# Kernel optimization log

Measured on AMD Instinct MI355X. Metric: run time of the kernel, lower is better.

## Reference

```python
import jax, jax.numpy as jnp
import numpy as np

B, L, C = 16, 4096, 32
D = 512
W = 24                  # rolling window
LAGS = [3, 5, 7]
MAXLEN = 5000
EPS = 1e-5


def setup_inputs() -> dict:
    key = jax.random.key(0)
    ks = jax.random.split(key, 8)
    return {
        "x": jax.random.normal(ks[0], (B, L, C), jnp.float32),
        "conv_w": jax.random.normal(ks[1], (D, C * (5 + len(LAGS)), 3), jnp.float32) * 0.05,
        "conv_b": jnp.zeros((D,), jnp.float32),
        "learned_pe": jax.random.normal(ks[2], (1, MAXLEN, D), jnp.float32) * (1.0 / np.sqrt(D)),
        "tape_pos": jax.random.normal(ks[3], (MAXLEN, D), jnp.float32) * 0.02,
        "tproj_w": jax.random.normal(ks[4], (D, D), jnp.float32) * 0.02,
        "tproj_b": jnp.zeros((D,), jnp.float32),
        "mixer_w": jax.random.normal(ks[5], (D, 2 * D), jnp.float32) * 0.02,
        "mixer_b": jnp.zeros((D,), jnp.float32),
        "g_c": jnp.ones((D,), jnp.float32), "b_c": jnp.zeros((D,), jnp.float32),
        "g_f": jnp.ones((D,), jnp.float32), "b_f": jnp.zeros((D,), jnp.float32),
        "g_l": jnp.ones((D,), jnp.float32), "b_l": jnp.zeros((D,), jnp.float32),
        "g_t": jnp.ones((D,), jnp.float32), "b_t": jnp.zeros((D,), jnp.float32),
        "weight_params": jnp.array([0.25, 0.25, 0.25, 0.25], jnp.float32),
    }


def _layer_norm(h, g, b):
    m = jnp.mean(h, axis=-1, keepdims=True)
    v = jnp.mean((h - m) ** 2, axis=-1, keepdims=True)
    return g * (h - m) / jnp.sqrt(v + EPS) + b


def reference(x, conv_w, conv_b, learned_pe, tape_pos, tproj_w, tproj_b,
              mixer_w, mixer_b, g_c, b_c, g_f, b_f, g_l, b_l, g_t, b_t,
              weight_params):
    Bx, Lx, Cx = x.shape
    # --- RollingFeatureExtractor: replicate-pad left, sliding mean/max/min/std
    xp = jnp.pad(x, ((0, 0), (W - 1, 0), (0, 0)), mode="edge")          # [B, L+W-1, C]
    win = jnp.stack([xp[:, i:i + Lx, :] for i in range(W)], axis=2)       # [B, L, W, C]
    w_mean = jnp.mean(win, axis=2)
    w_max = jnp.max(win, axis=2)
    w_min = jnp.min(win, axis=2)
    w_var = jnp.sum((win - w_mean[:, :, None, :]) ** 2, axis=2) / (W - 1)  # unbiased, torch.std default
    w_std = jnp.sqrt(w_var)
    x_stats = jnp.concatenate([x, w_mean, w_max, w_min, w_std], axis=-1)  # [B, L, 5C]
    # --- lag differences (replicate pad left by max lag)
    ml = max(LAGS)
    xl = jnp.pad(x, ((0, 0), (ml, 0), (0, 0)), mode="edge")
    x_lags = jnp.concatenate([x - xl[:, ml - l:ml - l + Lx, :] for l in LAGS], axis=-1)  # [B, L, 3C]
    comb = jnp.concatenate([x_stats, x_lags], axis=-1)                    # [B, L, 8C]
    # --- TokenEmbedding: Conv1d k=3, circular padding
    h = comb.transpose(0, 2, 1)                                           # [B, 8C, L]
    h = jnp.pad(h, ((0, 0), (0, 0), (1, 1)), mode="wrap")
    h = jax.lax.conv_general_dilated(h, conv_w, (1,), "VALID",
                                     dimension_numbers=("NCH", "OIH", "NCH"))
    h = h + conv_b[None, :, None]
    combined_emb = _layer_norm(h.transpose(0, 2, 1), g_c, b_c)            # [B, L, D]
    # --- fixed sinusoidal PE (constant / detached)
    pos = jnp.arange(Lx)
    div = jnp.exp(jnp.arange(0, D, 2).astype(x.dtype) * (-(np.log(10000.0) / D)))
    ang = pos[:, None].astype(x.dtype) * div[None, :]                     # [L, D/2]
    pe_fixed_tab = jnp.zeros((Lx, D), x.dtype).at[:, 0::2].set(jnp.sin(ang)).at[:, 1::2].set(jnp.cos(ang))
    pe_fixed = _layer_norm(pe_fixed_tab, g_f, b_f)[None]                  # [1, L, D]
    # --- learnable PE
    pe_learned = _layer_norm(learned_pe[:, :Lx], g_l, b_l)                # [1, L, D]
    # --- tAPE: token proj + learned pos embedding -> mixer linear
    pe = tape_pos[pos]                                                    # [L, D]
    tok = combined_emb @ tproj_w.T + tproj_b                              # [B, L, D]
    mixed = jnp.concatenate([tok, jnp.broadcast_to(pe[None], tok.shape)], axis=-1)
    pe_tape = _layer_norm(mixed @ mixer_w.T + mixer_b, g_t, b_t)          # [B, L, D]
    # --- softmax-weighted sum (dropout is identity in eval)
    w = jax.nn.softmax(weight_params)
    return (w[0] * combined_emb + w[1] * pe_fixed + w[2] * pe_learned + w[3] * pe_tape)
```

## Files before the change

kernel.cpp:

```cpp
#include <hip/hip_runtime.h>
#include <stdint.h>


typedef unsigned short u16;
using short8  = __attribute__((ext_vector_type(8))) short;
using floatx4 = __attribute__((ext_vector_type(4))) float;
typedef __attribute__((address_space(1))) const unsigned int u32_as1;
typedef __attribute__((address_space(3))) unsigned int       u32_as3;

static __device__ __forceinline__ u16 f2b(float f) {
  unsigned u = __float_as_uint(f);
  u += 0x7FFFu + ((u >> 16) & 1u);
  return (u16)(u >> 16);
}
static __device__ __forceinline__ float b2f(u16 h) {
  return __uint_as_float(((unsigned)h) << 16);
}

__global__ __launch_bounds__(256) void prep_all(
    const float* __restrict__ x,
    const float* __restrict__ conv_w, const float* __restrict__ mixer_w,
    const float* __restrict__ tproj_w, const float* __restrict__ tape_pos,
    const float* __restrict__ tproj_b, const float* __restrict__ mixer_b,
    const float* __restrict__ learned_pe,
    const float* __restrict__ gf, const float* __restrict__ bf_,
    const float* __restrict__ gl, const float* __restrict__ bl,
    const float* __restrict__ wp,
    u16* __restrict__ W1, u16* __restrict__ A_m1, u16* __restrict__ M2t,
    u16* __restrict__ tprojT, u16* __restrict__ tape_bf,
    float* __restrict__ bias2, u16* __restrict__ pw_tab,
    u16* __restrict__ comb) {
  __shared__ float sx[87 * 32];
  const int bx = blockIdx.x;
  if (bx < 12800) {
    int i = bx * 256 + threadIdx.x;
    if (i < 393216) {
      int d = i / 768, rem = i - d * 768;
      int j = rem >> 8, c = rem & 255;
      W1[i] = f2b(conv_w[(d * 256 + c) * 3 + j]);
    } else if (i < 393216 + 262144) {
      int k = i - 393216; int p = k >> 9, r = k & 511;
      A_m1[k] = f2b(mixer_w[p * 1024 + r]);
    } else if (i < 393216 + 524288) {
      int k = i - 393216 - 262144; int p = k >> 9, r = k & 511;
      M2t[k] = f2b(mixer_w[p * 1024 + 512 + r]);
    } else if (i < 393216 + 786432) {
      int k = i - 393216 - 524288; int q = k >> 9, r = k & 511;
      tprojT[k] = f2b(tproj_w[r * 512 + q]);
    } else if (i < 393216 + 786432 + 2097152) {
      int k = i - 393216 - 786432;
      tape_bf[k] = f2b(tape_pos[k]);
    }
    return;
  }
  if (bx < 12802) {
    int p = (bx - 12800) * 256 + threadIdx.x;
    if (p < 512) {
      float s = mixer_b[p];
      for (int r = 0; r < 512; ++r) s += mixer_w[p * 1024 + r] * tproj_b[r];
      bias2[p] = s;
    }
    return;
  }
  if (bx < 13826) {
    float a0 = wp[0], a1 = wp[1], a2 = wp[2], a3 = wp[3];
    float mxw = fmaxf(fmaxf(a0, a1), fmaxf(a2, a3));
    float e0 = expf(a0 - mxw), e1 = expf(a1 - mxw);
    float e2 = expf(a2 - mxw), e3 = expf(a3 - mxw);
    float invs = 1.f / (e0 + e1 + e2 + e3);
    float w1 = e1 * invs, w2 = e2 * invs;

    int row = (bx - 12802) * 4 + (threadIdx.x >> 6);
    int lane = threadIdx.x & 63;
    size_t base = (size_t)row * 512 + lane * 8;
    float v[8]; float s1 = 0.f, s2 = 0.f;
    #pragma unroll
    for (int e = 0; e < 8; ++e) {
      int d = lane * 8 + e;
      int de = d & ~1;
      float div = expf((float)de * (-9.210340371976184f / 512.f));
      float ang = (float)row * div;
      v[e] = (d & 1) ? cosf(ang) : sinf(ang);
      s1 += v[e]; s2 += v[e] * v[e];
    }
    #pragma unroll
    for (int off = 32; off; off >>= 1) { s1 += __shfl_xor(s1, off); s2 += __shfl_xor(s2, off); }
    float mean = s1 * (1.f / 512.f);
    float inv = rsqrtf(fmaxf(s2 * (1.f / 512.f) - mean * mean, 0.f) + 1e-5f);
    float pwv[8];
    #pragma unroll
    for (int e = 0; e < 8; ++e) {
      int d = lane * 8 + e;
      pwv[e] = w1 * (gf[d] * ((v[e] - mean) * inv) + bf_[d]);
    }
    const float4* lp = (const float4*)(learned_pe + base);
    float4 a = lp[0], bq = lp[1];
    float u[8] = {a.x, a.y, a.z, a.w, bq.x, bq.y, bq.z, bq.w};
    s1 = 0.f; s2 = 0.f;
    #pragma unroll
    for (int e = 0; e < 8; ++e) { s1 += u[e]; s2 += u[e] * u[e]; }
    #pragma unroll
    for (int off = 32; off; off >>= 1) { s1 += __shfl_xor(s1, off); s2 += __shfl_xor(s2, off); }
    mean = s1 * (1.f / 512.f);
    inv = rsqrtf(fmaxf(s2 * (1.f / 512.f) - mean * mean, 0.f) + 1e-5f);
    short8 o;
    #pragma unroll
    for (int e = 0; e < 8; ++e) {
      int d = lane * 8 + e;
      o[e] = (short)f2b(pwv[e] + w2 * (gl[d] * ((u[e] - mean) * inv) + bl[d]));
    }
    *(short8*)(pw_tab + base) = o;
    return;
  }
  const int fb = bx - 13826;
  const int b = fb >> 6, l0 = (fb & 63) * 64;
  for (int idx = threadIdx.x; idx < 87 * 32; idx += 256) {
    int r = idx >> 5, c = idx & 31;
    int ls = l0 - 23 + r; if (ls < 0) ls = 0;
    sx[idx] = x[((size_t)b * 4096 + ls) * 32 + c];
  }
  __syncthreads();
  const int c = threadIdx.x & 31, lr0 = threadIdx.x >> 5;
  for (int pass = 0; pass < 8; ++pass) {
    int lr = pass * 8 + lr0;
    int l = l0 + lr;
    float w[24];
    float s = 0.f, mx = -3.4e38f, mn = 3.4e38f;
    #pragma unroll
    for (int i = 0; i < 24; ++i) {
      float v = sx[(lr + i) * 32 + c];
      w[i] = v; s += v; mx = fmaxf(mx, v); mn = fminf(mn, v);
    }
    float mean = s * (1.f / 24.f);
    float ssd = 0.f;
    #pragma unroll
    for (int i = 0; i < 24; ++i) { float d = w[i] - mean; ssd += d * d; }
    float sd = sqrtf(fmaxf(ssd, 0.f) * (1.f / 23.f));
    float xv = w[23];
    float lag3 = xv - sx[(lr + 20) * 32 + c];
    float lag5 = xv - sx[(lr + 18) * 32 + c];
    float lag7 = xv - sx[(lr + 16) * 32 + c];
    size_t base = ((size_t)b * 4096 + l) * 256 + c;
    comb[base +   0] = f2b(xv);
    comb[base +  32] = f2b(mean);
    comb[base +  64] = f2b(mx);
    comb[base +  96] = f2b(mn);
    comb[base + 128] = f2b(sd);
    comb[base + 160] = f2b(lag3);
    comb[base + 192] = f2b(lag5);
    comb[base + 224] = f2b(lag7);
  }
}

static __device__ __forceinline__ void gemm_bt_dev(
    const u16* __restrict__ A, const u16* __restrict__ Bt,
    u16* __restrict__ outp, int K, int ldc,
    const float* __restrict__ bias, int m0, int n0,
    u16* lA, u16* lB) {
  const int tid = threadIdx.x;
  const int wave = tid >> 6, lane = tid & 63;
  const int wm = (wave & 1) * 64, wn = (wave >> 1) * 64;
  const int quad = lane >> 4, r16 = lane & 15;
  const int rowT = tid >> 3, col8 = tid & 7;

  floatx4 acc[4][4];
  #pragma unroll
  for (int i = 0; i < 4; ++i)
    #pragma unroll
    for (int j = 0; j < 4; ++j) acc[i][j] = (floatx4){0.f, 0.f, 0.f, 0.f};

  for (int kk = 0; kk < K; kk += 64) {
    __syncthreads();
    #pragma unroll
    for (int it = 0; it < 4; ++it) {
      int rr = it * 32 + rowT;
      const u16* ga = A  + (size_t)(m0 + rr) * K + kk + col8 * 8;
      const u16* gb = Bt + (size_t)(n0 + rr) * K + kk + col8 * 8;
      __builtin_amdgcn_global_load_lds((u32_as1*)ga, (u32_as3*)&lA[rr * 64 + col8 * 8], 16, 0, 0);
      __builtin_amdgcn_global_load_lds((u32_as1*)gb, (u32_as3*)&lB[rr * 64 + col8 * 8], 16, 0, 0);
    }
    __syncthreads();
    #pragma unroll
    for (int ks = 0; ks < 64; ks += 32) {
      short8 af[4], bfr[4];
      #pragma unroll
      for (int i = 0; i < 4; ++i)
        af[i] = *(const short8*)&lA[(wm + i * 16 + r16) * 64 + ks + quad * 8];
      #pragma unroll
      for (int j = 0; j < 4; ++j)
        bfr[j] = *(const short8*)&lB[(wn + j * 16 + r16) * 64 + ks + quad * 8];
      #pragma unroll
      for (int i = 0; i < 4; ++i)
        #pragma unroll
        for (int j = 0; j < 4; ++j)
          acc[i][j] = __builtin_amdgcn_mfma_f32_16x16x32_bf16(af[i], bfr[j], acc[i][j], 0, 0, 0);
    }
  }
  #pragma unroll
  for (int i = 0; i < 4; ++i) {
    #pragma unroll
    for (int rr = 0; rr < 4; ++rr) {
      int m = m0 + wm + i * 16 + quad * 4 + rr;
      #pragma unroll
      for (int j = 0; j < 4; ++j) {
        int n = n0 + wn + j * 16 + r16;
        float v = acc[i][j][rr];
        if (bias) v += bias[n];
        outp[(size_t)m * ldc + n] = f2b(v);
      }
    }
  }
}

__global__ __launch_bounds__(256) void gemm_bt_both(
    const u16* __restrict__ A_m1, const u16* __restrict__ tprojT,
    u16* __restrict__ Wf, const u16* __restrict__ tape_bf,
    const u16* __restrict__ M2t, u16* __restrict__ ctab_bf,
    const float* __restrict__ bias2) {
  __shared__ __align__(16) u16 lA[128 * 64];
  __shared__ __align__(16) u16 lB[128 * 64];
  const int bx = blockIdx.x;
  if (bx < 16) {
    gemm_bt_dev(A_m1, tprojT, Wf, 512, 512, nullptr,
                (bx & 3) * 128, (bx >> 2) * 128, lA, lB);
  } else {
    const int i = bx - 16;
    gemm_bt_dev(tape_bf, M2t, ctab_bf, 512, 512, bias2,
                (i & 31) * 128, (i >> 5) * 128, lA, lB);
  }
}


#define STAGE_A(SRCEXPR)                                                       \
  _Pragma("unroll")                                                            \
  for (int it = 0; it < 2; ++it) {                                             \
    int id = it * 256 + tid, row = id >> 3, c = id & 7;                        \
    int cg = ((c ^ (row & 7)) << 3);                                           \
    const u16* gsrc = (SRCEXPR);                                               \
    __builtin_amdgcn_global_load_lds((u32_as1*)gsrc,                           \
        (u32_as3*)(smem + id * 16), 16, 0, 0);                                 \
  }
#define STAGE_B(SRCEXPR)                                                       \
  _Pragma("unroll")                                                            \
  for (int it = 0; it < 16; ++it) {                                            \
    int id = it * 256 + tid, row = id >> 3, c = id & 7;                        \
    int cg = ((c ^ (row & 7)) << 3);                                           \
    const u16* gsrc = (SRCEXPR);                                               \
    __builtin_amdgcn_global_load_lds((u32_as1*)gsrc,                           \
        (u32_as3*)(smem + 8192 + id * 16), 16, 0, 0);                          \
  }

__global__ __launch_bounds__(256, 2) void gemm_conv_pre(
    const u16* __restrict__ comb, const u16* __restrict__ W1,
    const float* __restrict__ conv_b, const float* __restrict__ g_c,
    const float* __restrict__ b_c, const u16* __restrict__ Wf,
    const u16* __restrict__ ctab_bf, const u16* __restrict__ pw_tab,
    const float* __restrict__ g_t, const float* __restrict__ b_t,
    const float* __restrict__ wp,
    u16* __restrict__ ce, float* __restrict__ out) {
  __shared__ __align__(16) char smem[73728];
  __shared__ __align__(16) float sGB[1024];
  float* sG = sGB;
  float* sB = sGB + 512;
  u16* lA = (u16*)smem;
  u16* lB = (u16*)(smem + 8192);
  u16* lT = (u16*)smem;

  const int tid = threadIdx.x;
  if (tid < 128) {
    ((float4*)sG)[tid] = ((const float4*)g_c)[tid];
    ((float4*)sB)[tid] = ((const float4*)b_c)[tid];
  }
  const int m0 = blockIdx.x * 64;
  const int b = m0 >> 12, l0 = m0 & 4095;
  const int w = tid >> 6, lane = tid & 63;
  const int quad = lane >> 4, r16 = lane & 15;
  const int wn = w * 128;

  floatx4 acc[4][8];
  #pragma unroll
  for (int i = 0; i < 4; ++i)
    #pragma unroll
    for (int jj = 0; jj < 8; ++jj) acc[i][jj] = (floatx4){0.f, 0.f, 0.f, 0.f};

  for (int kk = 0; kk < 768; kk += 64) {
    const int jsh = kk >> 8, kc = kk & 255;
    __syncthreads();
    STAGE_A(comb + (((size_t)b * 4096 + ((l0 + row + jsh - 1 + 4096) & 4095)) << 8) + kc + cg)
    STAGE_B(W1 + (size_t)row * 768 + kk + cg)
    __syncthreads();
    #pragma unroll
    for (int ks = 0; ks < 64; ks += 32) {
      short8 af[4];
      #pragma unroll
      for (int i = 0; i < 4; ++i) {
        int row = i * 16 + r16;
        af[i] = *(const short8*)&lA[row * 64 + ((((ks >> 3) + quad) ^ (row & 7)) << 3)];
      }
      #pragma unroll
      for (int jj = 0; jj < 8; ++jj) {
        int row = wn + jj * 16 + r16;
        short8 bf = *(const short8*)&lB[row * 64 + ((((ks >> 3) + quad) ^ (row & 7)) << 3)];
        #pragma unroll
        for (int i = 0; i < 4; ++i)
          acc[i][jj] = __builtin_amdgcn_mfma_f32_16x16x32_bf16(bf, af[i], acc[i][jj], 0, 0, 0);
      }
    }
  }
  __syncthreads();
  #pragma unroll
  for (int jj = 0; jj < 8; ++jj) {
    int n = wn + jj * 16 + quad * 4;
    float4 b4 = *(const float4*)&conv_b[n];
    #pragma unroll
    for (int i = 0; i < 4; ++i) {
      ushort4 pk;
      pk.x = f2b(acc[i][jj][0] + b4.x);
      pk.y = f2b(acc[i][jj][1] + b4.y);
      pk.z = f2b(acc[i][jj][2] + b4.z);
      pk.w = f2b(acc[i][jj][3] + b4.w);
      *(ushort4*)(lT + (size_t)(i * 16 + r16) * 520 + n) = pk;
    }
  }
  __syncthreads();
  {
    const int orow = tid >> 2, part = tid & 3;
    u16* rowp = lT + (size_t)orow * 520;
    float s1 = 0.f, s2 = 0.f;
    #pragma unroll
    for (int k = 0; k < 16; ++k) {
      short8 t8 = *(const short8*)(rowp + (part + k * 4) * 8);
      #pragma unroll
      for (int e = 0; e < 8; ++e) {
        float f = b2f((u16)t8[e]); s1 += f; s2 += f * f;
      }
    }
    s1 += __shfl_xor(s1, 1); s2 += __shfl_xor(s2, 1);
    s1 += __shfl_xor(s1, 2); s2 += __shfl_xor(s2, 2);
    float mean = s1 * (1.f / 512.f);
    float inv = rsqrtf(fmaxf(s2 * (1.f / 512.f) - mean * mean, 0.f) + 1e-5f);
    size_t mrow = (size_t)(m0 + orow) * 512;
    #pragma unroll
    for (int k = 0; k < 16; ++k) {
      int c8 = part + k * 4;
      short8 t8 = *(const short8*)(rowp + c8 * 8);
      short8 o;
      #pragma unroll
      for (int e = 0; e < 8; ++e) {
        int d = c8 * 8 + e;
        o[e] = (short)f2b(sG[d] * ((b2f((u16)t8[e]) - mean) * inv) + sB[d]);
      }
      *(short8*)(ce + mrow + c8 * 8) = o;
    }
  }
  __syncthreads();
  if (tid < 128) {
    ((float4*)sG)[tid] = ((const float4*)g_t)[tid];
    ((float4*)sB)[tid] = ((const float4*)b_t)[tid];
  }

  floatx4 acc2[4][8];
  #pragma unroll
  for (int i = 0; i < 4; ++i)
    #pragma unroll
    for (int jj = 0; jj < 8; ++jj) acc2[i][jj] = (floatx4){0.f, 0.f, 0.f, 0.f};

  for (int kk = 0; kk < 512; kk += 64) {
    __syncthreads();
    STAGE_A(ce + (size_t)(m0 + row) * 512 + kk + cg)
    STAGE_B(Wf + (size_t)row * 512 + kk + cg)
    __syncthreads();
    #pragma unroll
    for (int ks = 0; ks < 64; ks += 32) {
      short8 af[4];
      #pragma unroll
      for (int i = 0; i < 4; ++i) {
        int row = i * 16 + r16;
        af[i] = *(const short8*)&lA[row * 64 + ((((ks >> 3) + quad) ^ (row & 7)) << 3)];
      }
      #pragma unroll
      for (int jj = 0; jj < 8; ++jj) {
        int row = wn + jj * 16 + r16;
        short8 bf = *(const short8*)&lB[row * 64 + ((((ks >> 3) + quad) ^ (row & 7)) << 3)];
        #pragma unroll
        for (int i = 0; i < 4; ++i)
          acc2[i][jj] = __builtin_amdgcn_mfma_f32_16x16x32_bf16(bf, af[i], acc2[i][jj], 0, 0, 0);
      }
    }
  }
  __syncthreads();
  #pragma unroll
  for (int jj = 0; jj < 8; ++jj) {
    int n = wn + jj * 16 + quad * 4;
    #pragma unroll
    for (int i = 0; i < 4; ++i) {
      ushort4 pk;
      pk.x = f2b(acc2[i][jj][0]);
      pk.y = f2b(acc2[i][jj][1]);
      pk.z = f2b(acc2[i][jj][2]);
      pk.w = f2b(acc2[i][jj][3]);
      *(ushort4*)(lT + (size_t)(i * 16 + r16) * 520 + n) = pk;
    }
  }
  __syncthreads();
  const int orow = tid >> 2, part = tid & 3;
  const int m = m0 + orow, l = l0 + orow;
  const u16* rowp = lT + (size_t)orow * 520;
  const size_t lrow = (size_t)l * 512, mrow = (size_t)m * 512;
  float s1 = 0.f, s2 = 0.f;
  #pragma unroll
  for (int k = 0; k < 16; ++k) {
    int c8 = part + k * 4;
    short8 t8 = *(const short8*)(rowp + c8 * 8);
    short8 ct = *(const short8*)(ctab_bf + lrow + c8 * 8);
    #pragma unroll
    for (int e = 0; e < 8; ++e) {
      float f = b2f((u16)t8[e]) + b2f((u16)ct[e]);
      s1 += f; s2 += f * f;
    }
  }
  s1 += __shfl_xor(s1, 1); s2 += __shfl_xor(s2, 1);
  s1 += __shfl_xor(s1, 2); s2 += __shfl_xor(s2, 2);
  float mean = s1 * (1.f / 512.f);
  float inv = rsqrtf(fmaxf(s2 * (1.f / 512.f) - mean * mean, 0.f) + 1e-5f);

  float a0 = wp[0], a1 = wp[1], a2 = wp[2], a3 = wp[3];
  float mxw = fmaxf(fmaxf(a0, a1), fmaxf(a2, a3));
  float e0 = expf(a0 - mxw), e1 = expf(a1 - mxw), e2 = expf(a2 - mxw), e3 = expf(a3 - mxw);
  float invs = 1.f / (e0 + e1 + e2 + e3);
  float w0 = e0 * invs, w3 = e3 * invs;

  #pragma unroll
  for (int k = 0; k < 16; ++k) {
    int c8 = part + k * 4;
    short8 t8  = *(const short8*)(rowp + c8 * 8);
    short8 ct  = *(const short8*)(ctab_bf + lrow + c8 * 8);
    short8 c8v = *(const short8*)(ce + mrow + c8 * 8);
    short8 pw  = *(const short8*)(pw_tab + lrow + c8 * 8);
    float o[8];
    #pragma unroll
    for (int e = 0; e < 8; ++e) {
      int d = c8 * 8 + e;
      float f = b2f((u16)t8[e]) + b2f((u16)ct[e]);
      float pt = sG[d] * ((f - mean) * inv) + sB[d];
      o[e] = w0 * b2f((u16)c8v[e]) + b2f((u16)pw[e]) + w3 * pt;
    }
    float4* op = (float4*)(out + mrow + c8 * 8);
    op[0] = make_float4(o[0], o[1], o[2], o[3]);
    op[1] = make_float4(o[4], o[5], o[6], o[7]);
  }
}

extern "C" void kernel_launch(void* const* d_in, const int* in_sizes, int n_in,
                              void* d_out, int out_size, void* d_ws, size_t ws_size,
                              hipStream_t stream) {
  const float* x          = (const float*)d_in[0];
  const float* conv_w     = (const float*)d_in[1];
  const float* conv_b     = (const float*)d_in[2];
  const float* learned_pe = (const float*)d_in[3];
  const float* tape_pos   = (const float*)d_in[4];
  const float* tproj_w    = (const float*)d_in[5];
  const float* tproj_b    = (const float*)d_in[6];
  const float* mixer_w    = (const float*)d_in[7];
  const float* mixer_b    = (const float*)d_in[8];
  const float* g_c        = (const float*)d_in[9];
  const float* b_c        = (const float*)d_in[10];
  const float* g_f        = (const float*)d_in[11];
  const float* b_f        = (const float*)d_in[12];
  const float* g_l        = (const float*)d_in[13];
  const float* b_l        = (const float*)d_in[14];
  const float* g_t        = (const float*)d_in[15];
  const float* b_t        = (const float*)d_in[16];
  const float* wp         = (const float*)d_in[17];

  char* ws = (char*)d_ws;
  u16*  comb    = (u16*)(ws + 0);
  u16*  ce      = (u16*)(ws + 33554432);
  char* S       = ws + 100663296;
  u16*  W1      = (u16*)(S + 0);
  u16*  A_m1    = (u16*)(S + 786432);
  u16*  M2t     = (u16*)(S + 1310720);
  u16*  tprojT  = (u16*)(S + 1835008);
  u16*  tape_bf = (u16*)(S + 2359296);
  u16*  Wf      = (u16*)(S + 6553600);
  u16*  ctab_bf = (u16*)(S + 7077888);
  float* bias2  = (float*)(S + 11272192);
  u16*  pw_tab  = (u16*)(S + 11274240);

  prep_all<<<14850, 256, 0, stream>>>(x, conv_w, mixer_w, tproj_w, tape_pos,
                                      tproj_b, mixer_b, learned_pe,
                                      g_f, b_f, g_l, b_l, wp,
                                      W1, A_m1, M2t, tprojT, tape_bf,
                                      bias2, pw_tab, comb);
  gemm_bt_both<<<144, 256, 0, stream>>>(A_m1, tprojT, Wf, tape_bf, M2t,
                                        ctab_bf, bias2);
  gemm_conv_pre<<<1024, 256, 0, stream>>>(comb, W1, conv_b, g_c, b_c,
                                          Wf, ctab_bf, pw_tab,
                                          g_t, b_t, wp, ce, (float*)d_out);
}
```

Measured before the change: 351.4 us.

## Double-buffer weight tiles with async LDS prefetch and 128-row tiles in fused GEMM

Reworks the fused conv/tAPE GEMM kernel to use 512-thread blocks covering 128 rows, with two waves along M. The shared weight tile is loaded once per block instead of once per 64 rows. The K loop becomes a software pipeline: the weight operand is double-buffered and the next A/B tiles are prefetched through global_load_lds with explicit vmcnt waits and raw barriers. MFMA sections also raise wave priority. The epilogues process the two 64-row halves in turn through shared memory. The cost is a much larger LDS footprint (about 144 KB), which limits residency to one block per CU, plus more barriers in the epilogue.

```diff
diff --git a/kernel.cpp b/kernel.cpp
--- a/kernel.cpp
+++ b/kernel.cpp
@@ -231,26 +231,30 @@
 }
 
 
-#define STAGE_A(SRCEXPR)                                                       \
+#define STAGE_A5(SRCEXPR)                                                      \
   _Pragma("unroll")                                                            \
   for (int it = 0; it < 2; ++it) {                                             \
-    int id = it * 256 + tid, row = id >> 3, c = id & 7;                        \
+    int id = it * 512 + tid, row = id >> 3, c = id & 7;                        \
     int cg = ((c ^ (row & 7)) << 3);                                           \
     const u16* gsrc = (SRCEXPR);                                               \
     __builtin_amdgcn_global_load_lds((u32_as1*)gsrc,                           \
         (u32_as3*)(smem + id * 16), 16, 0, 0);                                 \
   }
-#define STAGE_B(SRCEXPR)                                                       \
+#define STAGE_B5(BUFOFF, SRCEXPR)                                              \
   _Pragma("unroll")                                                            \
-  for (int it = 0; it < 16; ++it) {                                            \
-    int id = it * 256 + tid, row = id >> 3, c = id & 7;                        \
+  for (int it = 0; it < 8; ++it) {                                             \
+    int id = it * 512 + tid, row = id >> 3, c = id & 7;                        \
     int cg = ((c ^ (row & 7)) << 3);                                           \
     const u16* gsrc = (SRCEXPR);                                               \
     __builtin_amdgcn_global_load_lds((u32_as1*)gsrc,                           \
-        (u32_as3*)(smem + 8192 + id * 16), 16, 0, 0);                          \
-  }
-
-__global__ __launch_bounds__(256, 2) void gemm_conv_pre(
+        (u32_as3*)(smem + (BUFOFF) + id * 16), 16, 0, 0);                      \
+  }
+#define RAW_BARRIER()                                                          \
+  __builtin_amdgcn_sched_barrier(0);                                           \
+  __builtin_amdgcn_s_barrier();                                                \
+  __builtin_amdgcn_sched_barrier(0);
+
+__global__ __launch_bounds__(512, 2) void gemm_conv_pre(
     const u16* __restrict__ comb, const u16* __restrict__ W1,
     const float* __restrict__ conv_b, const float* __restrict__ g_c,
     const float* __restrict__ b_c, const u16* __restrict__ Wf,
@@ -258,78 +262,97 @@
     const float* __restrict__ g_t, const float* __restrict__ b_t,
     const float* __restrict__ wp,
     u16* __restrict__ ce, float* __restrict__ out) {
-  __shared__ __align__(16) char smem[73728];
-  __shared__ __align__(16) float sGB[1024];
-  float* sG = sGB;
-  float* sB = sGB + 512;
-  u16* lA = (u16*)smem;
-  u16* lB = (u16*)(smem + 8192);
-  u16* lT = (u16*)smem;
+  __shared__ __align__(16) char smem[147456];
+  u16*   lA = (u16*)smem;
+  u16*   lT = (u16*)smem;
+  float* sG = (float*)(smem + 67584);
+  float* sB = (float*)(smem + 69632);
 
   const int tid = threadIdx.x;
+  const int m0 = blockIdx.x * 128;
+  const int b = m0 >> 12, l0 = m0 & 4095;
+  const int w = tid >> 6, lane = tid & 63;
+  const int quad = lane >> 4, r16 = lane & 15;
+  const int wm2 = w >> 2, wn = (w & 3) * 128;
+
+  floatx4 acc[4][8];
+  #pragma unroll
+  for (int i = 0; i < 4; ++i)
+    #pragma unroll
+    for (int jj = 0; jj < 8; ++jj) acc[i][jj] = (floatx4){0.f, 0.f, 0.f, 0.f};
+
+  STAGE_A5(comb + (((size_t)b * 4096 + ((l0 + row - 1 + 4096) & 4095)) << 8) + cg)
+  STAGE_B5(16384, W1 + (size_t)row * 768 + 0 + cg)
+  STAGE_B5(81920, W1 + (size_t)row * 768 + 64 + cg)
+
+  for (int t = 0; t < 12; ++t) {
+    __builtin_amdgcn_sched_barrier(0);
+    if (t + 1 < 12) {
+      asm volatile("s_waitcnt vmcnt(8)" ::: "memory");
+    } else {
+      asm volatile("s_waitcnt vmcnt(0)" ::: "memory");
+    }
+    RAW_BARRIER();
+    const u16* lBc = (const u16*)(smem + 16384 + (t & 1) * 65536);
+    #pragma unroll
+    for (int ks = 0; ks < 64; ks += 32) {
+      short8 af[4];
+      #pragma unroll
+      for (int i = 0; i < 4; ++i) {
+        int row = wm2 * 64 + i * 16 + r16;
+        af[i] = *(const short8*)&lA[row * 64 + ((((ks >> 3) + quad) ^ (row & 7)) << 3)];
+      }
+      __builtin_amdgcn_s_setprio(1);
+      #pragma unroll
+      for (int jj = 0; jj < 8; ++jj) {
+        int row = wn + jj * 16 + r16;
+        short8 bf = *(const short8*)&lBc[row * 64 + ((((ks >> 3) + quad) ^ (row & 7)) << 3)];
+        #pragma unroll
+        for (int i = 0; i < 4; ++i)
+          acc[i][jj] = __builtin_amdgcn_mfma_f32_16x16x32_bf16(bf, af[i], acc[i][jj], 0, 0, 0);
+      }
+      __builtin_amdgcn_s_setprio(0);
+    }
+    RAW_BARRIER();
+    if (t + 1 < 12) {
+      const int kk1 = (t + 1) * 64;
+      const int jsh1 = kk1 >> 8, kc1 = kk1 & 255;
+      STAGE_A5(comb + (((size_t)b * 4096 + ((l0 + row + jsh1 - 1 + 4096) & 4095)) << 8) + kc1 + cg)
+    }
+    if (t + 2 < 12) {
+      STAGE_B5(16384 + (t & 1) * 65536, W1 + (size_t)row * 768 + (t + 2) * 64 + cg)
+    }
+  }
+  __syncthreads();
   if (tid < 128) {
     ((float4*)sG)[tid] = ((const float4*)g_c)[tid];
     ((float4*)sB)[tid] = ((const float4*)b_c)[tid];
   }
-  const int m0 = blockIdx.x * 64;
-  const int b = m0 >> 12, l0 = m0 & 4095;
-  const int w = tid >> 6, lane = tid & 63;
-  const int quad = lane >> 4, r16 = lane & 15;
-  const int wn = w * 128;
-
-  floatx4 acc[4][8];
+  const int orow = tid >> 3, part = tid & 7;
   #pragma unroll
-  for (int i = 0; i < 4; ++i)
-    #pragma unroll
-    for (int jj = 0; jj < 8; ++jj) acc[i][jj] = (floatx4){0.f, 0.f, 0.f, 0.f};
-
-  for (int kk = 0; kk < 768; kk += 64) {
-    const int jsh = kk >> 8, kc = kk & 255;
+  for (int h = 0; h < 2; ++h) {
+    if (wm2 == h) {
+      #pragma unroll
+      for (int jj = 0; jj < 8; ++jj) {
+        int n = wn + jj * 16 + quad * 4;
+        float4 b4 = *(const float4*)&conv_b[n];
+        #pragma unroll
+        for (int i = 0; i < 4; ++i) {
+          ushort4 pk;
+          pk.x = f2b(acc[i][jj][0] + b4.x);
+          pk.y = f2b(acc[i][jj][1] + b4.y);
+          pk.z = f2b(acc[i][jj][2] + b4.z);
+          pk.w = f2b(acc[i][jj][3] + b4.w);
+          *(ushort4*)(lT + (size_t)(i * 16 + r16) * 520 + n) = pk;
+        }
+      }
+    }
     __syncthreads();
-    STAGE_A(comb + (((size_t)b * 4096 + ((l0 + row + jsh - 1 + 4096) & 4095)) << 8) + kc + cg)
-    STAGE_B(W1 + (size_t)row * 768 + kk + cg)
-    __syncthreads();
-    #pragma unroll
-    for (int ks = 0; ks < 64; ks += 32) {
-      short8 af[4];
-      #pragma unroll
-      for (int i = 0; i < 4; ++i) {
-        int row = i * 16 + r16;
-        af[i] = *(const short8*)&lA[row * 64 + ((((ks >> 3) + quad) ^ (row & 7)) << 3)];
-      }
-      #pragma unroll
-      for (int jj = 0; jj < 8; ++jj) {
-        int row = wn + jj * 16 + r16;
-        short8 bf = *(const short8*)&lB[row * 64 + ((((ks >> 3) + quad) ^ (row & 7)) << 3)];
-        #pragma unroll
-        for (int i = 0; i < 4; ++i)
-          acc[i][jj] = __builtin_amdgcn_mfma_f32_16x16x32_bf16(bf, af[i], acc[i][jj], 0, 0, 0);
-      }
-    }
-  }
-  __syncthreads();
-  #pragma unroll
-  for (int jj = 0; jj < 8; ++jj) {
-    int n = wn + jj * 16 + quad * 4;
-    float4 b4 = *(const float4*)&conv_b[n];
-    #pragma unroll
-    for (int i = 0; i < 4; ++i) {
-      ushort4 pk;
-      pk.x = f2b(acc[i][jj][0] + b4.x);
-      pk.y = f2b(acc[i][jj][1] + b4.y);
-      pk.z = f2b(acc[i][jj][2] + b4.z);
-      pk.w = f2b(acc[i][jj][3] + b4.w);
-      *(ushort4*)(lT + (size_t)(i * 16 + r16) * 520 + n) = pk;
-    }
-  }
-  __syncthreads();
-  {
-    const int orow = tid >> 2, part = tid & 3;
-    u16* rowp = lT + (size_t)orow * 520;
+    const u16* rowp = lT + (size_t)orow * 520;
     float s1 = 0.f, s2 = 0.f;
     #pragma unroll
-    for (int k = 0; k < 16; ++k) {
-      short8 t8 = *(const short8*)(rowp + (part + k * 4) * 8);
+    for (int k = 0; k < 8; ++k) {
+      short8 t8 = *(const short8*)(rowp + (part + k * 8) * 8);
       #pragma unroll
       for (int e = 0; e < 8; ++e) {
         float f = b2f((u16)t8[e]); s1 += f; s2 += f * f;
@@ -337,12 +360,13 @@
     }
     s1 += __shfl_xor(s1, 1); s2 += __shfl_xor(s2, 1);
     s1 += __shfl_xor(s1, 2); s2 += __shfl_xor(s2, 2);
+    s1 += __shfl_xor(s1, 4); s2 += __shfl_xor(s2, 4);
     float mean = s1 * (1.f / 512.f);
     float inv = rsqrtf(fmaxf(s2 * (1.f / 512.f) - mean * mean, 0.f) + 1e-5f);
-    size_t mrow = (size_t)(m0 + orow) * 512;
-    #pragma unroll
-    for (int k = 0; k < 16; ++k) {
-      int c8 = part + k * 4;
+    size_t mrow = (size_t)(m0 + h * 64 + orow) * 512;
+    #pragma unroll
+    for (int k = 0; k < 8; ++k) {
+      int c8 = part + k * 8;
       short8 t8 = *(const short8*)(rowp + c8 * 8);
       short8 o;
       #pragma unroll
@@ -351,6 +375,54 @@
         o[e] = (short)f2b(sG[d] * ((b2f((u16)t8[e]) - mean) * inv) + sB[d]);
       }
       *(short8*)(ce + mrow + c8 * 8) = o;
+    }
+    __syncthreads();
+  }
+
+  floatx4 acc2[4][8];
+  #pragma unroll
+  for (int i = 0; i < 4; ++i)
+    #pragma unroll
+    for (int jj = 0; jj < 8; ++jj) acc2[i][jj] = (floatx4){0.f, 0.f, 0.f, 0.f};
+
+  STAGE_A5(ce + (size_t)(m0 + row) * 512 + 0 + cg)
+  STAGE_B5(16384, Wf + (size_t)row * 512 + 0 + cg)
+  STAGE_B5(81920, Wf + (size_t)row * 512 + 64 + cg)
+
+  for (int t = 0; t < 8; ++t) {
+    __builtin_amdgcn_sched_barrier(0);
+    if (t + 1 < 8) {
+      asm volatile("s_waitcnt vmcnt(8)" ::: "memory");
+    } else {
+      asm volatile("s_waitcnt vmcnt(0)" ::: "memory");
+    }
+    RAW_BARRIER();
+    const u16* lBc = (const u16*)(smem + 16384 + (t & 1) * 65536);
+    #pragma unroll
+    for (int ks = 0; ks < 64; ks += 32) {
+      short8 af[4];
+      #pragma unroll
+      for (int i = 0; i < 4; ++i) {
+        int row = wm2 * 64 + i * 16 + r16;
+        af[i] = *(const short8*)&lA[row * 64 + ((((ks >> 3) + quad) ^ (row & 7)) << 3)];
+      }
+      __builtin_amdgcn_s_setprio(1);
+      #pragma unroll
+      for (int jj = 0; jj < 8; ++jj) {
+        int row = wn + jj * 16 + r16;
+        short8 bf = *(const short8*)&lBc[row * 64 + ((((ks >> 3) + quad) ^ (row & 7)) << 3)];
+        #pragma unroll
+        for (int i = 0; i < 4; ++i)
+          acc2[i][jj] = __builtin_amdgcn_mfma_f32_16x16x32_bf16(bf, af[i], acc2[i][jj], 0, 0, 0);
+      }
+      __builtin_amdgcn_s_setprio(0);
+    }
+    RAW_BARRIER();
+    if (t + 1 < 8) {
+      STAGE_A5(ce + (size_t)(m0 + row) * 512 + (t + 1) * 64 + cg)
+    }
+    if (t + 2 < 8) {
+      STAGE_B5(16384 + (t & 1) * 65536, Wf + (size_t)row * 512 + (t + 2) * 64 + cg)
     }
   }
   __syncthreads();
@@ -358,72 +430,6 @@
     ((float4*)sG)[tid] = ((const float4*)g_t)[tid];
     ((float4*)sB)[tid] = ((const float4*)b_t)[tid];
   }
-
-  floatx4 acc2[4][8];
-  #pragma unroll
-  for (int i = 0; i < 4; ++i)
-    #pragma unroll
-    for (int jj = 0; jj < 8; ++jj) acc2[i][jj] = (floatx4){0.f, 0.f, 0.f, 0.f};
-
-  for (int kk = 0; kk < 512; kk += 64) {
-    __syncthreads();
-    STAGE_A(ce + (size_t)(m0 + row) * 512 + kk + cg)
-    STAGE_B(Wf + (size_t)row * 512 + kk + cg)
-    __syncthreads();
-    #pragma unroll
-    for (int ks = 0; ks < 64; ks += 32) {
-      short8 af[4];
-      #pragma unroll
-      for (int i = 0; i < 4; ++i) {
-        int row = i * 16 + r16;
-        af[i] = *(const short8*)&lA[row * 64 + ((((ks >> 3) + quad) ^ (row & 7)) << 3)];
-      }
-      #pragma unroll
-      for (int jj = 0; jj < 8; ++jj) {
-        int row = wn + jj * 16 + r16;
-        short8 bf = *(const short8*)&lB[row * 64 + ((((ks >> 3) + quad) ^ (row & 7)) << 3)];
-        #pragma unroll
-        for (int i = 0; i < 4; ++i)
-          acc2[i][jj] = __builtin_amdgcn_mfma_f32_16x16x32_bf16(bf, af[i], acc2[i][jj], 0, 0, 0);
-      }
-    }
-  }
-  __syncthreads();
-  #pragma unroll
-  for (int jj = 0; jj < 8; ++jj) {
-    int n = wn + jj * 16 + quad * 4;
-    #pragma unroll
-    for (int i = 0; i < 4; ++i) {
-      ushort4 pk;
-      pk.x = f2b(acc2[i][jj][0]);
-      pk.y = f2b(acc2[i][jj][1]);
-      pk.z = f2b(acc2[i][jj][2]);
-      pk.w = f2b(acc2[i][jj][3]);
-      *(ushort4*)(lT + (size_t)(i * 16 + r16) * 520 + n) = pk;
-    }
-  }
-  __syncthreads();
-  const int orow = tid >> 2, part = tid & 3;
-  const int m = m0 + orow, l = l0 + orow;
-  const u16* rowp = lT + (size_t)orow * 520;
-  const size_t lrow = (size_t)l * 512, mrow = (size_t)m * 512;
-  float s1 = 0.f, s2 = 0.f;
-  #pragma unroll
-  for (int k = 0; k < 16; ++k) {
-    int c8 = part + k * 4;
-    short8 t8 = *(const short8*)(rowp + c8 * 8);
-    short8 ct = *(const short8*)(ctab_bf + lrow + c8 * 8);
-    #pragma unroll
-    for (int e = 0; e < 8; ++e) {
-      float f = b2f((u16)t8[e]) + b2f((u16)ct[e]);
-      s1 += f; s2 += f * f;
-    }
-  }
-  s1 += __shfl_xor(s1, 1); s2 += __shfl_xor(s2, 1);
-  s1 += __shfl_xor(s1, 2); s2 += __shfl_xor(s2, 2);
-  float mean = s1 * (1.f / 512.f);
-  float inv = rsqrtf(fmaxf(s2 * (1.f / 512.f) - mean * mean, 0.f) + 1e-5f);
-
   float a0 = wp[0], a1 = wp[1], a2 = wp[2], a3 = wp[3];
   float mxw = fmaxf(fmaxf(a0, a1), fmaxf(a2, a3));
   float e0 = expf(a0 - mxw), e1 = expf(a1 - mxw), e2 = expf(a2 - mxw), e3 = expf(a3 - mxw);
@@ -431,23 +437,64 @@
   float w0 = e0 * invs, w3 = e3 * invs;
 
   #pragma unroll
-  for (int k = 0; k < 16; ++k) {
-    int c8 = part + k * 4;
-    short8 t8  = *(const short8*)(rowp + c8 * 8);
-    short8 ct  = *(const short8*)(ctab_bf + lrow + c8 * 8);
-    short8 c8v = *(const short8*)(ce + mrow + c8 * 8);
-    short8 pw  = *(const short8*)(pw_tab + lrow + c8 * 8);
-    float o[8];
-    #pragma unroll
-    for (int e = 0; e < 8; ++e) {
-      int d = c8 * 8 + e;
-      float f = b2f((u16)t8[e]) + b2f((u16)ct[e]);
-      float pt = sG[d] * ((f - mean) * inv) + sB[d];
-      o[e] = w0 * b2f((u16)c8v[e]) + b2f((u16)pw[e]) + w3 * pt;
-    }
-    float4* op = (float4*)(out + mrow + c8 * 8);
-    op[0] = make_float4(o[0], o[1], o[2], o[3]);
-    op[1] = make_float4(o[4], o[5], o[6], o[7]);
+  for (int h = 0; h < 2; ++h) {
+    if (wm2 == h) {
+      #pragma unroll
+      for (int jj = 0; jj < 8; ++jj) {
+        int n = wn + jj * 16 + quad * 4;
+        #pragma unroll
+        for (int i = 0; i < 4; ++i) {
+          ushort4 pk;
+          pk.x = f2b(acc2[i][jj][0]);
+          pk.y = f2b(acc2[i][jj][1]);
+          pk.z = f2b(acc2[i][jj][2]);
+          pk.w = f2b(acc2[i][jj][3]);
+          *(ushort4*)(lT + (size_t)(i * 16 + r16) * 520 + n) = pk;
+        }
+      }
+    }
+    __syncthreads();
+    const int m = m0 + h * 64 + orow, l = l0 + h * 64 + orow;
+    const u16* rowp = lT + (size_t)orow * 520;
+    const size_t lrow = (size_t)l * 512, mrow = (size_t)m * 512;
+    float s1 = 0.f, s2 = 0.f;
+    #pragma unroll
+    for (int k = 0; k < 8; ++k) {
+      int c8 = part + k * 8;
+      short8 t8 = *(const short8*)(rowp + c8 * 8);
+      short8 ct = *(const short8*)(ctab_bf + lrow + c8 * 8);
+      #pragma unroll
+      for (int e = 0; e < 8; ++e) {
+        float f = b2f((u16)t8[e]) + b2f((u16)ct[e]);
+        s1 += f; s2 += f * f;
+      }
+    }
+    s1 += __shfl_xor(s1, 1); s2 += __shfl_xor(s2, 1);
+    s1 += __shfl_xor(s1, 2); s2 += __shfl_xor(s2, 2);
+    s1 += __shfl_xor(s1, 4); s2 += __shfl_xor(s2, 4);
+    float mean = s1 * (1.f / 512.f);
+    float inv = rsqrtf(fmaxf(s2 * (1.f / 512.f) - mean * mean, 0.f) + 1e-5f);
+
+    #pragma unroll
+    for (int k = 0; k < 8; ++k) {
+      int c8 = part + k * 8;
+      short8 t8  = *(const short8*)(rowp + c8 * 8);
+      short8 ct  = *(const short8*)(ctab_bf + lrow + c8 * 8);
+      short8 c8v = *(const short8*)(ce + mrow + c8 * 8);
+      short8 pw  = *(const short8*)(pw_tab + lrow + c8 * 8);
+      float o[8];
+      #pragma unroll
+      for (int e = 0; e < 8; ++e) {
+        int d = c8 * 8 + e;
+        float f = b2f((u16)t8[e]) + b2f((u16)ct[e]);
+        float pt = sG[d] * ((f - mean) * inv) + sB[d];
+        o[e] = w0 * b2f((u16)c8v[e]) + b2f((u16)pw[e]) + w3 * pt;
+      }
+      float4* op = (float4*)(out + mrow + c8 * 8);
+      op[0] = make_float4(o[0], o[1], o[2], o[3]);
+      op[1] = make_float4(o[4], o[5], o[6], o[7]);
+    }
+    __syncthreads();
   }
 }
 
@@ -494,7 +541,7 @@
                                       bias2, pw_tab, comb);
   gemm_bt_both<<<144, 256, 0, stream>>>(A_m1, tprojT, Wf, tape_bf, M2t,
                                         ctab_bf, bias2);
-  gemm_conv_pre<<<1024, 256, 0, stream>>>(comb, W1, conv_b, g_c, b_c,
-                                          Wf, ctab_bf, pw_tab,
-                                          g_t, b_t, wp, ce, (float*)d_out);
-}
+  gemm_conv_pre<<<512, 512, 0, stream>>>(comb, W1, conv_b, g_c, b_c,
+                                         Wf, ctab_bf, pw_tab,
+                                         g_t, b_t, wp, ce, (float*)d_out);
+}
```

Result: slower. 371.5 us (+5.7%).
